# Kernel tuning notes

Measured on AMD Instinct MI355X. Metric: run time of the kernel, lower is better.

The kernel has to match this reference:

```python
import jax, jax.numpy as jnp
import numpy as np

NEG = -100000.0  # matches torch masked_fill constant

def setup_inputs() -> dict:
    key = jax.random.key(0)
    k1, k2, k3, k4 = jax.random.split(key, 4)
    B, T, D, H, S = 8, 2048, 1024, 8, 128
    features = jax.random.normal(k1, (B, T, D), dtype=jnp.float32)
    begins = jax.random.randint(k2, (B, S), 0, 2016, dtype=jnp.int64)
    widths = jax.random.randint(k3, (B, S), 1, 33, dtype=jnp.int64)
    ends = jnp.minimum(begins + widths, T)
    key_w = jax.random.normal(k4, (H, D), dtype=jnp.float32) / np.sqrt(D)
    key_b = jnp.zeros((H,), dtype=jnp.float32)
    return {"features": features, "begins": begins, "ends": ends,
            "key_w": key_w, "key_b": key_b}


def reference(features, begins, ends, key_w, key_b):
    # features: [B, T, D]; begins/ends: [B, S]
    B, T, D = features.shape
    H = key_w.shape[0]
    S = begins.shape[1]
    pos = jnp.arange(T)  # [T]
    # span mask [B, S, T]
    mask = (begins[..., None] <= pos) & (pos < ends[..., None])
    # key projection: [B, T, H]
    logits = jnp.einsum('btd,hd->bth', features, key_w) + key_b
    # masked softmax over T per (batch, span, head): [B, S, T, H]
    masked = jnp.where(mask[..., None], logits[:, None, :, :], NEG)
    weights = jax.nn.softmax(masked, axis=-2)
    # values = features reshaped to heads: [B, T, H, D//H]
    values = features.reshape(B, T, H, D // H)
    res = jnp.einsum('bthd,bsth->bshd', values, weights)  # [B, S, H, D//H]
    return res.reshape(B, S, D)
```

## Files before the change

kernel.cpp:

```cpp
#include <hip/hip_runtime.h>

#define B_  8
#define T_  2048
#define D_  1024
#define H_  8
#define S_  128
#define NSPAN (B_ * S_)
#define NBLK  512


__global__ void init_counter(unsigned int* __restrict__ c) { *c = 0u; }

__global__ __launch_bounds__(512) void span_pool_v3(
    const float* __restrict__ feat,
    const int* __restrict__ begins,
    const int* __restrict__ ends,
    const float* __restrict__ kw,
    const float* __restrict__ kb,
    float* __restrict__ out,
    unsigned int* __restrict__ counter)
{
    const int wv   = threadIdx.x >> 6;
    const int lane = threadIdx.x & 63;

    __shared__ __align__(16) float kwl[H_ * D_];
    __shared__ __align__(16) float wts[32 * H_];
    __shared__ unsigned int s_span;

    {
        const float4* src = (const float4*)kw;
        float4*       dst = (float4*)kwl;
        dst[threadIdx.x]        = src[threadIdx.x];
        dst[threadIdx.x + 512]  = src[threadIdx.x + 512];
        dst[threadIdx.x + 1024] = src[threadIdx.x + 1024];
        dst[threadIdx.x + 1536] = src[threadIdx.x + 1536];
    }

    const float kbv = (lane < H_) ? kb[lane] : 0.f;

    for (;;) {
        if (threadIdx.x == 0) s_span = atomicAdd(counter, 1u);
        __syncthreads();
        const int s = (int)s_span;
        if (s >= NSPAN) break;

        const int begin = begins[s];
        const int width = ends[s] - begin;
        const size_t row0 = (size_t)(s >> 7) * T_ + begin;

        for (int r = wv; r < width; r += 8) {
            const float* fr = feat + (row0 + r) * D_ + lane * 4;
            float4 fv0 = *(const float4*)(fr +   0);
            float4 fv1 = *(const float4*)(fr + 256);
            float4 fv2 = *(const float4*)(fr + 512);
            float4 fv3 = *(const float4*)(fr + 768);

            float acc[H_];
#pragma unroll
            for (int h = 0; h < H_; ++h) {
                const float* kh = &kwl[h * D_ + lane * 4];
                float4 k0 = *(const float4*)(kh +   0);
                float4 k1 = *(const float4*)(kh + 256);
                float4 k2 = *(const float4*)(kh + 512);
                float4 k3 = *(const float4*)(kh + 768);
                acc[h] = fv0.x*k0.x + fv0.y*k0.y + fv0.z*k0.z + fv0.w*k0.w
                       + fv1.x*k1.x + fv1.y*k1.y + fv1.z*k1.z + fv1.w*k1.w
                       + fv2.x*k2.x + fv2.y*k2.y + fv2.z*k2.z + fv2.w*k2.w
                       + fv3.x*k3.x + fv3.y*k3.y + fv3.z*k3.z + fv3.w*k3.w;
            }
#pragma unroll
            for (int st = 0; st < 3; ++st) {
                const int mm = 1 << st;
                const bool hb = (lane >> st) & 1;
#pragma unroll
                for (int j = 0; j < (4 >> st); ++j) {
                    float mine  = hb ? acc[2*j + 1] : acc[2*j];
                    float other = hb ? acc[2*j]     : acc[2*j + 1];
                    acc[j] = mine + __shfl_xor(other, mm, 64);
                }
            }
            acc[0] += __shfl_xor(acc[0],  8, 64);
            acc[0] += __shfl_xor(acc[0], 16, 64);
            acc[0] += __shfl_xor(acc[0], 32, 64);

            if (lane < H_)
                wts[r * H_ + lane] = acc[0] + kbv;
        }
        __syncthreads();

        if (threadIdx.x < 64) {
            float4 lv = *(const float4*)&wts[lane * 4];
            const int w8 = width * H_;
            float v0 = (4 * lane + 0 < w8) ? lv.x : -1e30f;
            float v1 = (4 * lane + 1 < w8) ? lv.y : -1e30f;
            float v2 = (4 * lane + 2 < w8) ? lv.z : -1e30f;
            float v3 = (4 * lane + 3 < w8) ? lv.w : -1e30f;

            float m0 = v0, m1 = v1, m2 = v2, m3 = v3;
#pragma unroll
            for (int off = 2; off <= 32; off <<= 1) {
                m0 = fmaxf(m0, __shfl_xor(m0, off, 64));
                m1 = fmaxf(m1, __shfl_xor(m1, off, 64));
                m2 = fmaxf(m2, __shfl_xor(m2, off, 64));
                m3 = fmaxf(m3, __shfl_xor(m3, off, 64));
            }
            float e0 = __expf(v0 - m0);
            float e1 = __expf(v1 - m1);
            float e2 = __expf(v2 - m2);
            float e3 = __expf(v3 - m3);
            float s0 = e0, s1 = e1, s2 = e2, s3 = e3;
#pragma unroll
            for (int off = 2; off <= 32; off <<= 1) {
                s0 += __shfl_xor(s0, off, 64);
                s1 += __shfl_xor(s1, off, 64);
                s2 += __shfl_xor(s2, off, 64);
                s3 += __shfl_xor(s3, off, 64);
            }
            *(float4*)&wts[lane * 4] =
                make_float4(e0 / s0, e1 / s1, e2 / s2, e3 / s3);
        }
        __syncthreads();

        const int t  = threadIdx.x;
        const int ha = t >> 7;
        const float* fb = feat + row0 * D_;
        float a0 = 0.f, a1 = 0.f;
        for (int k = 0; k < width; ++k) {
            const float* frw = fb + (size_t)k * D_;
            a0 += wts[k * H_ + ha]     * frw[t];
            a1 += wts[k * H_ + ha + 4] * frw[t + 512];
        }
        out[(size_t)s * D_ + t]       = a0;
        out[(size_t)s * D_ + t + 512] = a1;
    }
}

extern "C" void kernel_launch(void* const* d_in, const int* in_sizes, int n_in,
                              void* d_out, int out_size, void* d_ws, size_t ws_size,
                              hipStream_t stream) {
    const float* feat   = (const float*)d_in[0];
    const int*   begins = (const int*)d_in[1];
    const int*   ends   = (const int*)d_in[2];
    const float* kw     = (const float*)d_in[3];
    const float* kb     = (const float*)d_in[4];
    float*       out    = (float*)d_out;
    unsigned int* counter = (unsigned int*)d_ws;

    init_counter<<<1, 1, 0, stream>>>(counter);
    span_pool_v3<<<NBLK, 512, 0, stream>>>(feat, begins, ends, kw, kb, out, counter);
}
```

Baseline: 116.4 us.

## Stage span rows in LDS and prefetch the next span's rows

The kernel now uses 1024-thread blocks with 16 waves, each covering two rows of a span, and half as many persistent blocks. Feature rows are copied into a shared row buffer so the weighted-sum pass reads them from LDS instead of loading them from global memory a second time. Rows for the next span are loaded into registers before the softmax and pooling of the current span, overlapping global latency with compute. The cost is about 160KB of shared memory per block, which limits residency to one block per CU, plus higher register pressure from holding two prefetched rows.

```diff
diff --git a/kernel.cpp b/kernel.cpp
--- a/kernel.cpp
+++ b/kernel.cpp
@@ -6,12 +6,47 @@
 #define H_  8
 #define S_  128
 #define NSPAN (B_ * S_)
-#define NBLK  512
+#define NBLK  256
+#define RBROWS 31
 
 
 __global__ void init_counter(unsigned int* __restrict__ c) { *c = 0u; }
 
-__global__ __launch_bounds__(512) void span_pool_v3(
+__device__ __forceinline__ void dot_row(const float* kwl, float* wts,
+                                        int r, int lane, float kbv,
+                                        float4 f0, float4 f1, float4 f2, float4 f3)
+{
+    float acc[H_];
+#pragma unroll
+    for (int h = 0; h < H_; ++h) {
+        const float* kh = &kwl[h * D_ + lane * 4];
+        float4 k0 = *(const float4*)(kh +   0);
+        float4 k1 = *(const float4*)(kh + 256);
+        float4 k2 = *(const float4*)(kh + 512);
+        float4 k3 = *(const float4*)(kh + 768);
+        acc[h] = f0.x*k0.x + f0.y*k0.y + f0.z*k0.z + f0.w*k0.w
+               + f1.x*k1.x + f1.y*k1.y + f1.z*k1.z + f1.w*k1.w
+               + f2.x*k2.x + f2.y*k2.y + f2.z*k2.z + f2.w*k2.w
+               + f3.x*k3.x + f3.y*k3.y + f3.z*k3.z + f3.w*k3.w;
+    }
+#pragma unroll
+    for (int st = 0; st < 3; ++st) {
+        const int mm = 1 << st;
+        const bool hb = (lane >> st) & 1;
+#pragma unroll
+        for (int j = 0; j < (4 >> st); ++j) {
+            float mine  = hb ? acc[2*j + 1] : acc[2*j];
+            float other = hb ? acc[2*j]     : acc[2*j + 1];
+            acc[j] = mine + __shfl_xor(other, mm, 64);
+        }
+    }
+    acc[0] += __shfl_xor(acc[0],  8, 64);
+    acc[0] += __shfl_xor(acc[0], 16, 64);
+    acc[0] += __shfl_xor(acc[0], 32, 64);
+    if (lane < H_) wts[r * H_ + lane] = acc[0] + kbv;
+}
+
+__global__ __launch_bounds__(1024, 4) void span_pool_v4(
     const float* __restrict__ feat,
     const int* __restrict__ begins,
     const int* __restrict__ ends,
@@ -20,75 +55,88 @@
     float* __restrict__ out,
     unsigned int* __restrict__ counter)
 {
-    const int wv   = threadIdx.x >> 6;
-    const int lane = threadIdx.x & 63;
+    const int tid  = threadIdx.x;
+    const int wv   = tid >> 6;
+    const int lane = tid & 63;
 
     __shared__ __align__(16) float kwl[H_ * D_];
+    __shared__ __align__(16) float rowbuf[RBROWS * D_];
     __shared__ __align__(16) float wts[32 * H_];
     __shared__ unsigned int s_span;
 
     {
         const float4* src = (const float4*)kw;
         float4*       dst = (float4*)kwl;
-        dst[threadIdx.x]        = src[threadIdx.x];
-        dst[threadIdx.x + 512]  = src[threadIdx.x + 512];
-        dst[threadIdx.x + 1024] = src[threadIdx.x + 1024];
-        dst[threadIdx.x + 1536] = src[threadIdx.x + 1536];
+        dst[tid]        = src[tid];
+        dst[tid + 1024] = src[tid + 1024];
     }
 
     const float kbv = (lane < H_) ? kb[lane] : 0.f;
 
-    for (;;) {
-        if (threadIdx.x == 0) s_span = atomicAdd(counter, 1u);
+    if (tid == 0) s_span = atomicAdd(counter, 1u);
+    __syncthreads();
+    int s = (int)s_span;
+    bool have = (s < NSPAN);
+
+    int width = 0;
+    size_t row0 = 0;
+    float4 fA0, fA1, fA2, fA3, fB0, fB1, fB2, fB3;
+
+    if (have) {
+        const int begin = begins[s];
+        width = ends[s] - begin;
+        row0  = (size_t)(s >> 7) * T_ + begin;
+        if (wv < width) {
+            const float* fr = feat + (row0 + wv) * D_ + lane * 4;
+            fA0 = *(const float4*)(fr +   0); fA1 = *(const float4*)(fr + 256);
+            fA2 = *(const float4*)(fr + 512); fA3 = *(const float4*)(fr + 768);
+        }
+        if (wv + 16 < width) {
+            const float* fr = feat + (row0 + wv + 16) * D_ + lane * 4;
+            fB0 = *(const float4*)(fr +   0); fB1 = *(const float4*)(fr + 256);
+            fB2 = *(const float4*)(fr + 512); fB3 = *(const float4*)(fr + 768);
+        }
+    }
+
+    while (have) {
+        if (wv < width) {
+            float* rb = &rowbuf[wv * D_ + lane * 4];
+            *(float4*)(rb +   0) = fA0;  *(float4*)(rb + 256) = fA1;
+            *(float4*)(rb + 512) = fA2;  *(float4*)(rb + 768) = fA3;
+            dot_row(kwl, wts, wv, lane, kbv, fA0, fA1, fA2, fA3);
+        }
+        if (wv + 16 < width) {
+            if (wv + 16 < RBROWS) {
+                float* rb = &rowbuf[(wv + 16) * D_ + lane * 4];
+                *(float4*)(rb +   0) = fB0;  *(float4*)(rb + 256) = fB1;
+                *(float4*)(rb + 512) = fB2;  *(float4*)(rb + 768) = fB3;
+            }
+            dot_row(kwl, wts, wv + 16, lane, kbv, fB0, fB1, fB2, fB3);
+        }
+
+        if (tid == 0) s_span = atomicAdd(counter, 1u);
         __syncthreads();
-        const int s = (int)s_span;
-        if (s >= NSPAN) break;
+        const int snext = (int)s_span;
+        const bool havenext = (snext < NSPAN);
+        int width_n = 0;
+        size_t row0_n = 0;
+        if (havenext) {
+            const int begin_n = begins[snext];
+            width_n = ends[snext] - begin_n;
+            row0_n  = (size_t)(snext >> 7) * T_ + begin_n;
+            if (wv < width_n) {
+                const float* fr = feat + (row0_n + wv) * D_ + lane * 4;
+                fA0 = *(const float4*)(fr +   0); fA1 = *(const float4*)(fr + 256);
+                fA2 = *(const float4*)(fr + 512); fA3 = *(const float4*)(fr + 768);
+            }
+            if (wv + 16 < width_n) {
+                const float* fr = feat + (row0_n + wv + 16) * D_ + lane * 4;
+                fB0 = *(const float4*)(fr +   0); fB1 = *(const float4*)(fr + 256);
+                fB2 = *(const float4*)(fr + 512); fB3 = *(const float4*)(fr + 768);
+            }
+        }
 
-        const int begin = begins[s];
-        const int width = ends[s] - begin;
-        const size_t row0 = (size_t)(s >> 7) * T_ + begin;
-
-        for (int r = wv; r < width; r += 8) {
-            const float* fr = feat + (row0 + r) * D_ + lane * 4;
-            float4 fv0 = *(const float4*)(fr +   0);
-            float4 fv1 = *(const float4*)(fr + 256);
-            float4 fv2 = *(const float4*)(fr + 512);
-            float4 fv3 = *(const float4*)(fr + 768);
-
-            float acc[H_];
-#pragma unroll
-            for (int h = 0; h < H_; ++h) {
-                const float* kh = &kwl[h * D_ + lane * 4];
-                float4 k0 = *(const float4*)(kh +   0);
-                float4 k1 = *(const float4*)(kh + 256);
-                float4 k2 = *(const float4*)(kh + 512);
-                float4 k3 = *(const float4*)(kh + 768);
-                acc[h] = fv0.x*k0.x + fv0.y*k0.y + fv0.z*k0.z + fv0.w*k0.w
-                       + fv1.x*k1.x + fv1.y*k1.y + fv1.z*k1.z + fv1.w*k1.w
-                       + fv2.x*k2.x + fv2.y*k2.y + fv2.z*k2.z + fv2.w*k2.w
-                       + fv3.x*k3.x + fv3.y*k3.y + fv3.z*k3.z + fv3.w*k3.w;
-            }
-#pragma unroll
-            for (int st = 0; st < 3; ++st) {
-                const int mm = 1 << st;
-                const bool hb = (lane >> st) & 1;
-#pragma unroll
-                for (int j = 0; j < (4 >> st); ++j) {
-                    float mine  = hb ? acc[2*j + 1] : acc[2*j];
-                    float other = hb ? acc[2*j]     : acc[2*j + 1];
-                    acc[j] = mine + __shfl_xor(other, mm, 64);
-                }
-            }
-            acc[0] += __shfl_xor(acc[0],  8, 64);
-            acc[0] += __shfl_xor(acc[0], 16, 64);
-            acc[0] += __shfl_xor(acc[0], 32, 64);
-
-            if (lane < H_)
-                wts[r * H_ + lane] = acc[0] + kbv;
-        }
-        __syncthreads();
-
-        if (threadIdx.x < 64) {
+        if (tid < 64) {
             float4 lv = *(const float4*)&wts[lane * 4];
             const int w8 = width * H_;
             float v0 = (4 * lane + 0 < w8) ? lv.x : -1e30f;
@@ -121,17 +169,17 @@
         }
         __syncthreads();
 
-        const int t  = threadIdx.x;
-        const int ha = t >> 7;
-        const float* fb = feat + row0 * D_;
-        float a0 = 0.f, a1 = 0.f;
-        for (int k = 0; k < width; ++k) {
-            const float* frw = fb + (size_t)k * D_;
-            a0 += wts[k * H_ + ha]     * frw[t];
-            a1 += wts[k * H_ + ha + 4] * frw[t + 512];
-        }
-        out[(size_t)s * D_ + t]       = a0;
-        out[(size_t)s * D_ + t + 512] = a1;
+        const int ha = tid >> 7;
+        float a0 = 0.f;
+        const int wlim = (width < RBROWS) ? width : RBROWS;
+        for (int k = 0; k < wlim; ++k)
+            a0 += wts[k * H_ + ha] * rowbuf[k * D_ + tid];
+        if (width == 32)
+            a0 += wts[31 * H_ + ha] * feat[(row0 + 31) * D_ + tid];
+        out[(size_t)s * D_ + tid] = a0;
+        __syncthreads();
+
+        s = snext; have = havenext; width = width_n; row0 = row0_n;
     }
 }
 
@@ -147,5 +195,5 @@
     unsigned int* counter = (unsigned int*)d_ws;
 
     init_counter<<<1, 1, 0, stream>>>(counter);
-    span_pool_v3<<<NBLK, 512, 0, stream>>>(feat, begins, ends, kw, kb, out, counter);
+    span_pool_v4<<<NBLK, 1024, 0, stream>>>(feat, begins, ends, kw, kb, out, counter);
 }
```

Result: no change. 115.3 us (-1.0%).

## Stage span rows in LDS with cross-span prefetch and register-resident key weights

Applied to the files above, without the earlier changes.

Blocks grow to 1024 threads, and each wave pair splits the row's columns and heads. The key-projection weights now live in registers instead of LDS. Span rows are loaded once into a 128KB LDS buffer, so the pooling pass reads from LDS instead of re-reading global memory. The next span's first rows are prefetched while softmax and pooling run, and the work-counter atomic is double-buffered. The trade-off is fewer, larger blocks with heavy LDS use, plus a launch-bounds hint that may force a tight VGPR budget and spill the register-held weights.

```diff
diff --git a/kernel.cpp b/kernel.cpp
--- a/kernel.cpp
+++ b/kernel.cpp
@@ -6,12 +6,12 @@
 #define H_  8
 #define S_  128
 #define NSPAN (B_ * S_)
-#define NBLK  512
+#define NBLK  256
 
 
 __global__ void init_counter(unsigned int* __restrict__ c) { *c = 0u; }
 
-__global__ __launch_bounds__(512) void span_pool_v3(
+__global__ __launch_bounds__(1024, 4) void span_pool_v5(
     const float* __restrict__ feat,
     const int* __restrict__ begins,
     const int* __restrict__ ends,
@@ -20,83 +20,136 @@
     float* __restrict__ out,
     unsigned int* __restrict__ counter)
 {
-    const int wv   = threadIdx.x >> 6;
-    const int lane = threadIdx.x & 63;
-
-    __shared__ __align__(16) float kwl[H_ * D_];
+    const int tid  = threadIdx.x;
+    const int wv   = tid >> 6;
+    const int lane = tid & 63;
+    const int w    = wv >> 1;
+    const int p    = wv & 1;
+    const int coff = p * 512 + lane * 4;
+
+    __shared__ __align__(16) float rowbuf[32 * D_];
     __shared__ __align__(16) float wts[32 * H_];
-    __shared__ unsigned int s_span;
-
-    {
-        const float4* src = (const float4*)kw;
-        float4*       dst = (float4*)kwl;
-        dst[threadIdx.x]        = src[threadIdx.x];
-        dst[threadIdx.x + 512]  = src[threadIdx.x + 512];
-        dst[threadIdx.x + 1024] = src[threadIdx.x + 1024];
-        dst[threadIdx.x + 1536] = src[threadIdx.x + 1536];
+    __shared__ unsigned int s_slot[2];
+
+    float4 kwr[4][4];
+#pragma unroll
+    for (int h = 0; h < 4; ++h)
+#pragma unroll
+        for (int c = 0; c < 4; ++c)
+            kwr[h][c] = *(const float4*)(kw + (size_t)(4*p + h) * D_ + c * 256 + lane * 4);
+
+    const float kbq = kb[4*p + (lane & 3)];
+
+    auto dot_slot = [&](int r, float4 ra, float4 rb) {
+        const float* rbo = &rowbuf[r * D_ + (p ? 0 : 512) + lane * 4];
+        float4 fo0 = *(const float4*)(rbo);
+        float4 fo1 = *(const float4*)(rbo + 256);
+        const float4 f0 = p ? fo0 : ra;
+        const float4 f1 = p ? fo1 : rb;
+        const float4 f2 = p ? ra  : fo0;
+        const float4 f3 = p ? rb  : fo1;
+        float acc[4];
+#pragma unroll
+        for (int h = 0; h < 4; ++h) {
+            acc[h] = f0.x*kwr[h][0].x + f0.y*kwr[h][0].y + f0.z*kwr[h][0].z + f0.w*kwr[h][0].w
+                   + f1.x*kwr[h][1].x + f1.y*kwr[h][1].y + f1.z*kwr[h][1].z + f1.w*kwr[h][1].w
+                   + f2.x*kwr[h][2].x + f2.y*kwr[h][2].y + f2.z*kwr[h][2].z + f2.w*kwr[h][2].w
+                   + f3.x*kwr[h][3].x + f3.y*kwr[h][3].y + f3.z*kwr[h][3].z + f3.w*kwr[h][3].w;
+        }
+        const bool hb = lane & 1;
+        float mine  = hb ? acc[1] : acc[0];
+        float other = hb ? acc[0] : acc[1];
+        float t0 = mine + __shfl_xor(other, 1, 64);
+        mine  = hb ? acc[3] : acc[2];
+        other = hb ? acc[2] : acc[3];
+        float t1 = mine + __shfl_xor(other, 1, 64);
+        const bool hb2 = (lane >> 1) & 1;
+        mine  = hb2 ? t1 : t0;
+        other = hb2 ? t0 : t1;
+        float r0 = mine + __shfl_xor(other, 2, 64);
+        r0 += __shfl_xor(r0,  4, 64);
+        r0 += __shfl_xor(r0,  8, 64);
+        r0 += __shfl_xor(r0, 16, 64);
+        r0 += __shfl_xor(r0, 32, 64);
+        if (lane < 4) wts[r * H_ + 4*p + lane] = r0 + kbq;
+    };
+
+    if (tid == 0) s_slot[0] = atomicAdd(counter, 1u);
+    __syncthreads();
+    int s = (int)s_slot[0];
+    bool have = (s < NSPAN);
+    int width = 0; size_t row0 = 0;
+    float4 pfa0, pfa1, pfb0, pfb1;
+    if (have) {
+        const int bg = begins[s];
+        width = ends[s] - bg;
+        row0  = (size_t)(s >> 7) * T_ + bg;
+        if (w < width) {
+            const float* fr = feat + (row0 + w) * D_ + coff;
+            pfa0 = *(const float4*)(fr); pfa1 = *(const float4*)(fr + 256);
+        }
+        if (w + 8 < width) {
+            const float* fr = feat + (row0 + w + 8) * D_ + coff;
+            pfb0 = *(const float4*)(fr); pfb1 = *(const float4*)(fr + 256);
+        }
     }
 
-    const float kbv = (lane < H_) ? kb[lane] : 0.f;
-
-    for (;;) {
-        if (threadIdx.x == 0) s_span = atomicAdd(counter, 1u);
-        __syncthreads();
-        const int s = (int)s_span;
-        if (s >= NSPAN) break;
-
-        const int begin = begins[s];
-        const int width = ends[s] - begin;
-        const size_t row0 = (size_t)(s >> 7) * T_ + begin;
-
-        for (int r = wv; r < width; r += 8) {
-            const float* fr = feat + (row0 + r) * D_ + lane * 4;
-            float4 fv0 = *(const float4*)(fr +   0);
-            float4 fv1 = *(const float4*)(fr + 256);
-            float4 fv2 = *(const float4*)(fr + 512);
-            float4 fv3 = *(const float4*)(fr + 768);
-
-            float acc[H_];
-#pragma unroll
-            for (int h = 0; h < H_; ++h) {
-                const float* kh = &kwl[h * D_ + lane * 4];
-                float4 k0 = *(const float4*)(kh +   0);
-                float4 k1 = *(const float4*)(kh + 256);
-                float4 k2 = *(const float4*)(kh + 512);
-                float4 k3 = *(const float4*)(kh + 768);
-                acc[h] = fv0.x*k0.x + fv0.y*k0.y + fv0.z*k0.z + fv0.w*k0.w
-                       + fv1.x*k1.x + fv1.y*k1.y + fv1.z*k1.z + fv1.w*k1.w
-                       + fv2.x*k2.x + fv2.y*k2.y + fv2.z*k2.z + fv2.w*k2.w
-                       + fv3.x*k3.x + fv3.y*k3.y + fv3.z*k3.z + fv3.w*k3.w;
-            }
-#pragma unroll
-            for (int st = 0; st < 3; ++st) {
-                const int mm = 1 << st;
-                const bool hb = (lane >> st) & 1;
-#pragma unroll
-                for (int j = 0; j < (4 >> st); ++j) {
-                    float mine  = hb ? acc[2*j + 1] : acc[2*j];
-                    float other = hb ? acc[2*j]     : acc[2*j + 1];
-                    acc[j] = mine + __shfl_xor(other, mm, 64);
-                }
-            }
-            acc[0] += __shfl_xor(acc[0],  8, 64);
-            acc[0] += __shfl_xor(acc[0], 16, 64);
-            acc[0] += __shfl_xor(acc[0], 32, 64);
-
-            if (lane < H_)
-                wts[r * H_ + lane] = acc[0] + kbv;
-        }
-        __syncthreads();
-
-        if (threadIdx.x < 64) {
+    int it = 0;
+    while (have) {
+        if (tid == 0) s_slot[(it + 1) & 1] = atomicAdd(counter, 1u);
+
+        float4 g2a, g2b, g3a, g3b;
+        const bool v2 = (w + 16) < width, v3 = (w + 24) < width;
+        if (v2) { const float* fr = feat + (row0 + w + 16) * D_ + coff;
+                  g2a = *(const float4*)(fr); g2b = *(const float4*)(fr + 256); }
+        if (v3) { const float* fr = feat + (row0 + w + 24) * D_ + coff;
+                  g3a = *(const float4*)(fr); g3b = *(const float4*)(fr + 256); }
+        if (w < width) {
+            float* rb = &rowbuf[w * D_ + coff];
+            *(float4*)(rb) = pfa0; *(float4*)(rb + 256) = pfa1;
+        }
+        if (w + 8 < width) {
+            float* rb = &rowbuf[(w + 8) * D_ + coff];
+            *(float4*)(rb) = pfb0; *(float4*)(rb + 256) = pfb1;
+        }
+        if (v2) { float* rb = &rowbuf[(w + 16) * D_ + coff];
+                  *(float4*)(rb) = g2a; *(float4*)(rb + 256) = g2b; }
+        if (v3) { float* rb = &rowbuf[(w + 24) * D_ + coff];
+                  *(float4*)(rb) = g3a; *(float4*)(rb + 256) = g3b; }
+        __syncthreads();
+
+        if (w < width)      dot_slot(w,      pfa0, pfa1);
+        if (w + 8 < width)  dot_slot(w + 8,  pfb0, pfb1);
+        if (v2)             dot_slot(w + 16, g2a, g2b);
+        if (v3)             dot_slot(w + 24, g3a, g3b);
+        __syncthreads();
+
+        const int snext = (int)s_slot[(it + 1) & 1];
+        const bool havenext = (snext < NSPAN);
+        int width_n = 0; size_t row0_n = 0;
+        if (havenext) {
+            const int bg = begins[snext];
+            width_n = ends[snext] - bg;
+            row0_n  = (size_t)(snext >> 7) * T_ + bg;
+            if (w < width_n) {
+                const float* fr = feat + (row0_n + w) * D_ + coff;
+                pfa0 = *(const float4*)(fr); pfa1 = *(const float4*)(fr + 256);
+            }
+            if (w + 8 < width_n) {
+                const float* fr = feat + (row0_n + w + 8) * D_ + coff;
+                pfb0 = *(const float4*)(fr); pfb1 = *(const float4*)(fr + 256);
+            }
+        }
+
+        if (tid < 64) {
             float4 lv = *(const float4*)&wts[lane * 4];
             const int w8 = width * H_;
             float v0 = (4 * lane + 0 < w8) ? lv.x : -1e30f;
             float v1 = (4 * lane + 1 < w8) ? lv.y : -1e30f;
-            float v2 = (4 * lane + 2 < w8) ? lv.z : -1e30f;
-            float v3 = (4 * lane + 3 < w8) ? lv.w : -1e30f;
-
-            float m0 = v0, m1 = v1, m2 = v2, m3 = v3;
+            float v2s = (4 * lane + 2 < w8) ? lv.z : -1e30f;
+            float v3s = (4 * lane + 3 < w8) ? lv.w : -1e30f;
+
+            float m0 = v0, m1 = v1, m2 = v2s, m3 = v3s;
 #pragma unroll
             for (int off = 2; off <= 32; off <<= 1) {
                 m0 = fmaxf(m0, __shfl_xor(m0, off, 64));
@@ -106,8 +159,8 @@
             }
             float e0 = __expf(v0 - m0);
             float e1 = __expf(v1 - m1);
-            float e2 = __expf(v2 - m2);
-            float e3 = __expf(v3 - m3);
+            float e2 = __expf(v2s - m2);
+            float e3 = __expf(v3s - m3);
             float s0 = e0, s1 = e1, s2 = e2, s3 = e3;
 #pragma unroll
             for (int off = 2; off <= 32; off <<= 1) {
@@ -121,17 +174,21 @@
         }
         __syncthreads();
 
-        const int t  = threadIdx.x;
-        const int ha = t >> 7;
-        const float* fb = feat + row0 * D_;
-        float a0 = 0.f, a1 = 0.f;
-        for (int k = 0; k < width; ++k) {
-            const float* frw = fb + (size_t)k * D_;
-            a0 += wts[k * H_ + ha]     * frw[t];
-            a1 += wts[k * H_ + ha + 4] * frw[t + 512];
-        }
-        out[(size_t)s * D_ + t]       = a0;
-        out[(size_t)s * D_ + t + 512] = a1;
+        if (tid < 256) {
+            const int ha = tid >> 5;
+            float4 a = make_float4(0.f, 0.f, 0.f, 0.f);
+#pragma unroll 4
+            for (int k = 0; k < width; ++k) {
+                const float4 rv = *(const float4*)&rowbuf[k * D_ + tid * 4];
+                const float wt = wts[k * H_ + ha];
+                a.x += wt * rv.x; a.y += wt * rv.y;
+                a.z += wt * rv.z; a.w += wt * rv.w;
+            }
+            *(float4*)(out + (size_t)s * D_ + tid * 4) = a;
+        }
+        __syncthreads();
+
+        s = snext; have = havenext; width = width_n; row0 = row0_n; ++it;
     }
 }
 
@@ -147,5 +204,5 @@
     unsigned int* counter = (unsigned int*)d_ws;
 
     init_counter<<<1, 1, 0, stream>>>(counter);
-    span_pool_v3<<<NBLK, 512, 0, stream>>>(feat, begins, ends, kw, kb, out, counter);
+    span_pool_v5<<<NBLK, 1024, 0, stream>>>(feat, begins, ends, kw, kb, out, counter);
 }
```

After: 130.2 us. 11.9% more time.
